# Optimization experiments

Hardware: AMD Instinct MI355X
Metric: run time of the kernel (lower is better)

The kernel has to match this reference:

```python
import jax, jax.numpy as jnp
import numpy as np

D_STATE = 64
HEADDIM = 64
D_CONV = 4
EPS = 1e-5


def _layernorm(x, w, b):
    m = jnp.mean(x, -1, keepdims=True)
    v = jnp.mean((x - m) ** 2, -1, keepdims=True)
    return (x - m) * jax.lax.rsqrt(v + EPS) * w + b


def _mamba2(x, W_in, conv_w, conv_b, dt_bias, A_log, Dh, rms_w, W_out):
    # Mamba2 (SSD) forward: in_proj -> causal depthwise conv + silu -> selective scan
    # -> gated RMSNorm -> out_proj.  ngroups=1, headdim=64, d_state=64.
    Bb, L, _ = x.shape
    d_inner = rms_w.shape[0]
    H = dt_bias.shape[0]
    P = d_inner // H
    conv_dim = d_inner + 2 * D_STATE
    zxbcdt = x @ W_in                                   # [B,L,2*d_inner+2*N+H]
    z = zxbcdt[..., :d_inner]
    xBC = zxbcdt[..., d_inner:d_inner + conv_dim]
    dt = zxbcdt[..., d_inner + conv_dim:]               # [B,L,H]
    # causal depthwise conv1d (kernel D_CONV) + bias + silu
    xpad = jnp.pad(xBC, ((0, 0), (D_CONV - 1, 0), (0, 0)))
    xBC = sum(conv_w[k] * xpad[:, k:k + L] for k in range(D_CONV)) + conv_b
    xBC = jax.nn.silu(xBC)
    xh = xBC[..., :d_inner].reshape(Bb, L, H, P)        # [B,L,H,P]
    Bm = xBC[..., d_inner:d_inner + D_STATE]            # [B,L,N]
    Cm = xBC[..., d_inner + D_STATE:]                   # [B,L,N]
    dt = jax.nn.softplus(dt + dt_bias)                  # [B,L,H]
    A = -jnp.exp(A_log)                                 # [H]
    da = jnp.exp(dt * A)                                # [B,L,H] discrete decay
    dtx = dt[..., None] * xh                            # [B,L,H,P]

    def step(h, inp):
        da_t, dtx_t, B_t, C_t = inp
        h = da_t[:, :, None, None] * h + jnp.einsum('bhp,bn->bhpn', dtx_t, B_t)
        y_t = jnp.einsum('bhpn,bn->bhp', h, C_t)
        return h, y_t

    h0 = jnp.zeros((Bb, H, P, D_STATE), x.dtype)
    _, y = jax.lax.scan(step, h0, (da.transpose(1, 0, 2), dtx.transpose(1, 0, 2, 3),
                                   Bm.transpose(1, 0, 2), Cm.transpose(1, 0, 2)))
    y = y.transpose(1, 0, 2, 3) + Dh[None, None, :, None] * xh   # skip term
    y = y.reshape(Bb, L, d_inner)
    # gated RMSNorm (norm_before_gate=False): rmsnorm(y * silu(z)) * weight
    y = y * jax.nn.silu(z)
    y = y * jax.lax.rsqrt(jnp.mean(y * y, -1, keepdims=True) + EPS) * rms_w
    return y @ W_out


def _mamba_params(key, d_model, pre):
    d_inner = 2 * d_model
    H = d_inner // HEADDIM
    conv_dim = d_inner + 2 * D_STATE
    d_in = 2 * d_inner + 2 * D_STATE + H
    k = jax.random.split(key, 5)
    return {
        pre + '_W_in': jax.random.normal(k[0], (d_model, d_in), jnp.float32) * (d_model ** -0.5),
        pre + '_conv_w': jax.random.normal(k[1], (D_CONV, conv_dim), jnp.float32) * 0.2,
        pre + '_conv_b': jnp.zeros((conv_dim,), jnp.float32),
        pre + '_dt_bias': jnp.log(jnp.expm1(jax.random.uniform(k[2], (H,), jnp.float32, 0.001, 0.1))),
        pre + '_A_log': jnp.log(jax.random.uniform(k[3], (H,), jnp.float32, 1.0, 16.0)),
        pre + '_D': jnp.ones((H,), jnp.float32),
        pre + '_rms_w': jnp.ones((d_inner,), jnp.float32),
        pre + '_W_out': jax.random.normal(k[4], (d_inner, d_model), jnp.float32) * (d_inner ** -0.5),
    }


def setup_inputs() -> dict:
    key = jax.random.key(0)
    ks = jax.random.split(key, 3)
    B, L, C = 8, 1024, 128
    inp = {'x': jax.random.normal(ks[0], (B, L, C), jnp.float32)}
    inp['ln_spa_w'] = jnp.ones((C,), jnp.float32)
    inp['ln_spa_b'] = jnp.zeros((C,), jnp.float32)
    inp['ln_spe_w'] = jnp.ones((L,), jnp.float32)
    inp['ln_spe_b'] = jnp.zeros((L,), jnp.float32)
    inp.update(_mamba_params(ks[1], C, 'spa'))
    inp.update(_mamba_params(ks[2], L, 'spe'))
    return inp


def reference(x, ln_spa_w, ln_spa_b, ln_spe_w, ln_spe_b,
              spa_W_in, spa_conv_w, spa_conv_b, spa_dt_bias, spa_A_log, spa_D, spa_rms_w, spa_W_out,
              spe_W_in, spe_conv_w, spe_conv_b, spe_dt_bias, spe_A_log, spe_D, spe_rms_w, spe_W_out):
    # SSD_Block.forward (drop_path=0 -> identity)
    x_spa = _layernorm(x, ln_spa_w, ln_spa_b)
    x_spa = _mamba2(x_spa, spa_W_in, spa_conv_w, spa_conv_b, spa_dt_bias,
                    spa_A_log, spa_D, spa_rms_w, spa_W_out) + x
    x_spe = x_spa.transpose(0, 2, 1)                      # [B,C,L]
    x_spe = _layernorm(x_spe, ln_spe_w, ln_spe_b)
    x_spe = _mamba2(x_spe, spe_W_in, spe_conv_w, spe_conv_b, spe_dt_bias,
                    spe_A_log, spe_D, spe_rms_w, spe_W_out)
    return x_spe.transpose(0, 2, 1) + x_spa
```

## Files before the change

### kernel.cpp

```cpp
#include <hip/hip_runtime.h>
#include <hip/hip_bf16.h>

#define EPSV 1e-5f

typedef __attribute__((ext_vector_type(8))) short short8v;
typedef __attribute__((ext_vector_type(4))) float f32x4;

__device__ inline unsigned short f2bf(float f) {
  __hip_bfloat16 h = __float2bfloat16(f);
  return *reinterpret_cast<unsigned short*>(&h);
}

__device__ inline float bf2f(unsigned short u) {
  return __uint_as_float(((unsigned int)u) << 16);
}

__device__ inline float siluf(float x) { return x / (1.f + expf(-x)); }

__device__ inline void gload_lds16(const void* g, void* l) {
  __builtin_amdgcn_global_load_lds(
      (const __attribute__((address_space(1))) void*)g,
      (__attribute__((address_space(3))) void*)l, 16, 0, 0);
}

__device__ inline float block_sum(float v, float* lds) {
  #pragma unroll
  for (int o = 32; o; o >>= 1) v += __shfl_xor(v, o);
  int tid = threadIdx.x;
  if ((tid & 63) == 0) lds[tid >> 6] = v;
  __syncthreads();
  float r = lds[0] + lds[1] + lds[2] + lds[3];
  __syncthreads();
  return r;
}

__device__ inline float wave_prefix_incl(float v, int lane) {
  #pragma unroll
  for (int o = 1; o < 64; o <<= 1) {
    float u = __shfl_up(v, o);
    if (lane >= o) v += u;
  }
  return v;
}

__device__ inline void wtconv_tile(const float* __restrict__ W,
                                   unsigned short* __restrict__ Wt,
                                   int K, int N, int bx, int by) {
  __shared__ float tile[64][65];
  int n0 = bx * 64, k0 = by * 64;
  int tid = threadIdx.x;
  int r = tid >> 4, c4 = (tid & 15) * 4;
  #pragma unroll
  for (int i = 0; i < 4; i++) {
    int kk = r + i * 16;
    float4 v = make_float4(0.f, 0.f, 0.f, 0.f);
    if (n0 + c4 < N) v = *reinterpret_cast<const float4*>(&W[(long)(k0 + kk) * N + n0 + c4]);
    tile[kk][c4] = v.x; tile[kk][c4 + 1] = v.y; tile[kk][c4 + 2] = v.z; tile[kk][c4 + 3] = v.w;
  }
  __syncthreads();
  #pragma unroll
  for (int i = 0; i < 4; i++) {
    int nl = r + i * 16;
    if (n0 + nl < N) {
      ushort4 o;
      o.x = f2bf(tile[c4 + 0][nl]);
      o.y = f2bf(tile[c4 + 1][nl]);
      o.z = f2bf(tile[c4 + 2][nl]);
      o.w = f2bf(tile[c4 + 3][nl]);
      *reinterpret_cast<ushort4*>(&Wt[(long)(n0 + nl) * K + k0 + c4]) = o;
    }
  }
}

__global__ __launch_bounds__(256) void ln_wt_fused(const float* __restrict__ x,
                                                   const float* __restrict__ w,
                                                   const float* __restrict__ bb,
                                                   unsigned short* __restrict__ outA,
                                                   const float* __restrict__ W0,
                                                   unsigned short* __restrict__ T0,
                                                   const float* __restrict__ W1,
                                                   unsigned short* __restrict__ T1,
                                                   const float* __restrict__ W2,
                                                   unsigned short* __restrict__ T2,
                                                   const float* __restrict__ W3,
                                                   unsigned short* __restrict__ T3) {
  int id = blockIdx.x;
  if (id < 4096) {
    int tid = threadIdx.x;
    __shared__ float lds[4];
    long row = (long)id * 2 + (tid >> 7);
    int lane = tid & 127;
    int base = (tid >> 7) << 1;
    float v = x[row * 128 + lane];
    float s = v;
    #pragma unroll
    for (int o = 32; o; o >>= 1) s += __shfl_xor(s, o);
    if ((tid & 63) == 0) lds[tid >> 6] = s;
    __syncthreads();
    float m = (lds[base] + lds[base + 1]) * (1.f / 128.f);
    float d = v - m;
    float q = d * d;
    #pragma unroll
    for (int o = 32; o; o >>= 1) q += __shfl_xor(q, o);
    __syncthreads();
    if ((tid & 63) == 0) lds[tid >> 6] = q;
    __syncthreads();
    float inv = rsqrtf((lds[base] + lds[base + 1]) * (1.f / 128.f) + EPSV);
    outA[row * 128 + lane] = f2bf(d * inv * w[lane] + bb[lane]);
  } else {
    id -= 4096;
    if (id < 22)        { int r = id;        wtconv_tile(W0, T0, 128,  644,  r % 11, r / 11); }
    else if (id < 30)   { int r = id - 22;   wtconv_tile(W1, T1, 256,  128,  r % 2,  r / 2); }
    else if (id < 1102) { int r = id - 30;   wtconv_tile(W2, T2, 1024, 4256, r % 67, r / 67); }
    else                { int r = id - 1102; wtconv_tile(W3, T3, 2048, 1024, r % 16, r / 16); }
  }
}

__global__ __launch_bounds__(256) void spe_normT(const float* __restrict__ xspa,
                                                 const float* __restrict__ part2,
                                                 const float* __restrict__ w,
                                                 const float* __restrict__ bb,
                                                 unsigned short* __restrict__ out) {
  __shared__ float tile[128][65];
  int c0 = blockIdx.x * 64, l0 = blockIdx.y * 128, b = blockIdx.z;
  int tid = threadIdx.x;
  int rr = tid >> 4, c4 = (tid & 15) * 4;
  #pragma unroll
  for (int p = 0; p < 8; p++) {
    int l = rr + p * 16;
    f32x4 v = *reinterpret_cast<const f32x4*>(
        &xspa[((long)b * 1024 + l0 + l) * 128 + c0 + c4]);
    tile[l][c4] = v[0]; tile[l][c4 + 1] = v[1];
    tile[l][c4 + 2] = v[2]; tile[l][c4 + 3] = v[3];
  }
  __syncthreads();
  int ch = tid >> 2, lq = tid & 3;
  int gc = c0 + ch;
  int bx = gc >> 6, cl = gc & 63;
  float ssum = 0.f, qsum = 0.f;
  #pragma unroll
  for (int sub = 0; sub < 16; sub++) {
    int by = b * 16 + sub;
    float2 pq = *reinterpret_cast<const float2*>(&part2[(((by * 2 + bx) * 64) + cl) * 2]);
    ssum += pq.x; qsum += pq.y;
  }
  float mm = ssum * (1.f / 1024.f);
  float rstd = rsqrtf(qsum * (1.f / 1024.f) - mm * mm + EPSV);
  #pragma unroll
  for (int j = 0; j < 8; j++) {
    int qidx = lq + j * 4;
    int l = qidx * 4;
    float4 wv = *reinterpret_cast<const float4*>(&w[l0 + l]);
    float4 bv = *reinterpret_cast<const float4*>(&bb[l0 + l]);
    ushort4 o;
    o.x = f2bf((tile[l + 0][ch] - mm) * rstd * wv.x + bv.x);
    o.y = f2bf((tile[l + 1][ch] - mm) * rstd * wv.y + bv.y);
    o.z = f2bf((tile[l + 2][ch] - mm) * rstd * wv.z + bv.z);
    o.w = f2bf((tile[l + 3][ch] - mm) * rstd * wv.w + bv.w);
    *reinterpret_cast<ushort4*>(&out[((long)b * 128 + c0 + ch) * 1024 + l0 + l]) = o;
  }
}

__global__ __launch_bounds__(256) void gemm128_split(const unsigned short* __restrict__ A,
                                                     const unsigned short* __restrict__ Bt,
                                                     unsigned short* __restrict__ zout,
                                                     float* __restrict__ o2,
                                                     float* __restrict__ o3,
                                                     int M, int N, int K,
                                                     int c1, int c2) {
  __shared__ unsigned short As[128 * 32];
  __shared__ unsigned short Bs[128 * 32];
  int tid = threadIdx.x;
  int lane = tid & 63, w = tid >> 6;
  int wr = (w >> 1) * 64, wc = (w & 1) * 64;
  int ln15 = lane & 15, kg = lane >> 4;
  int rowBase = blockIdx.y * 128, colBase = blockIdx.x * 128;
  int srow = w * 32 + (lane >> 2);
  int scol = (lane & 3) * 8;
  f32x4 acc[4][4] = {};
  for (int k0 = 0; k0 < K; k0 += 32) {
    gload_lds16(&A[(long)(rowBase + srow) * K + k0 + scol], &As[(w * 32) * 32]);
    gload_lds16(&A[(long)(rowBase + srow + 16) * K + k0 + scol], &As[(w * 32 + 16) * 32]);
    gload_lds16(&Bt[(long)(colBase + srow) * K + k0 + scol], &Bs[(w * 32) * 32]);
    gload_lds16(&Bt[(long)(colBase + srow + 16) * K + k0 + scol], &Bs[(w * 32 + 16) * 32]);
    __syncthreads();
    short8v af[4], bfr[4];
    #pragma unroll
    for (int mt = 0; mt < 4; mt++)
      af[mt] = *reinterpret_cast<const short8v*>(&As[(wr + mt * 16 + ln15) * 32 + kg * 8]);
    #pragma unroll
    for (int nt = 0; nt < 4; nt++)
      bfr[nt] = *reinterpret_cast<const short8v*>(&Bs[(wc + nt * 16 + ln15) * 32 + kg * 8]);
    #pragma unroll
    for (int mt = 0; mt < 4; mt++)
      #pragma unroll
      for (int nt = 0; nt < 4; nt++)
        acc[mt][nt] = __builtin_amdgcn_mfma_f32_16x16x32_bf16(af[mt], bfr[nt], acc[mt][nt], 0, 0, 0);
    __syncthreads();
  }
  #pragma unroll
  for (int mt = 0; mt < 4; mt++)
    #pragma unroll
    for (int nt = 0; nt < 4; nt++)
      #pragma unroll
      for (int q = 0; q < 4; q++) {
        int r = rowBase + wr + mt * 16 + kg * 4 + q;
        int c = colBase + wc + nt * 16 + ln15;
        if (c < N) {
          float v = acc[mt][nt][q];
          if (c < c1) zout[(long)r * c1 + c] = f2bf(v);
          else if (c < c2) o2[(long)r * (c2 - c1) + (c - c1)] = v;
          else o3[(long)r * (N - c2) + (c - c2)] = v;
        }
      }
}

template <int MODE>
__global__ __launch_bounds__(256) void gemm_mfma(const unsigned short* __restrict__ A,
                                                 const unsigned short* __restrict__ Bt,
                                                 const float* __restrict__ R,
                                                 float* __restrict__ out,
                                                 float* __restrict__ part2,
                                                 int M, int N, int K) {
  __shared__ unsigned short As[64 * 40];
  __shared__ unsigned short Bs[64 * 40];
  int tid = threadIdx.x;
  int lane = tid & 63, w = tid >> 6;
  int wr = (w >> 1) * 32, wc = (w & 1) * 32;
  int ln15 = lane & 15, kg = lane >> 4;
  int rowBase = blockIdx.y * 64, colBase = blockIdx.x * 64;
  int sm = tid >> 2, skb = (tid & 3) * 8;
  f32x4 acc[2][2] = {};
  for (int k0 = 0; k0 < K; k0 += 32) {
    {
      short8v av = *reinterpret_cast<const short8v*>(&A[(long)(rowBase + sm) * K + k0 + skb]);
      *reinterpret_cast<short8v*>(&As[sm * 40 + skb]) = av;
      int n = colBase + sm;
      short8v bv = {0, 0, 0, 0, 0, 0, 0, 0};
      if (n < N) bv = *reinterpret_cast<const short8v*>(&Bt[(long)n * K + k0 + skb]);
      *reinterpret_cast<short8v*>(&Bs[sm * 40 + skb]) = bv;
    }
    __syncthreads();
    short8v af[2], bfr[2];
    #pragma unroll
    for (int mt = 0; mt < 2; mt++)
      af[mt] = *reinterpret_cast<const short8v*>(&As[(wr + mt * 16 + ln15) * 40 + kg * 8]);
    #pragma unroll
    for (int nt = 0; nt < 2; nt++)
      bfr[nt] = *reinterpret_cast<const short8v*>(&Bs[(wc + nt * 16 + ln15) * 40 + kg * 8]);
    #pragma unroll
    for (int mt = 0; mt < 2; mt++)
      #pragma unroll
      for (int nt = 0; nt < 2; nt++)
        acc[mt][nt] = __builtin_amdgcn_mfma_f32_16x16x32_bf16(af[mt], bfr[nt], acc[mt][nt], 0, 0, 0);
    __syncthreads();
  }
  if (MODE == 1) {
    float sC[2] = {0.f, 0.f}, qC[2] = {0.f, 0.f};
    #pragma unroll
    for (int mt = 0; mt < 2; mt++)
      #pragma unroll
      for (int nt = 0; nt < 2; nt++)
        #pragma unroll
        for (int q = 0; q < 4; q++) {
          int r = rowBase + wr + mt * 16 + kg * 4 + q;
          int c = colBase + wc + nt * 16 + ln15;
          float v = acc[mt][nt][q] + R[(long)r * N + c];
          out[(long)r * N + c] = v;
          sC[nt] += v;
          qC[nt] += v * v;
        }
    __shared__ float redS[4][32], redQ[4][32];
    #pragma unroll
    for (int nt = 0; nt < 2; nt++) {
      sC[nt] += __shfl_xor(sC[nt], 16);
      sC[nt] += __shfl_xor(sC[nt], 32);
      qC[nt] += __shfl_xor(qC[nt], 16);
      qC[nt] += __shfl_xor(qC[nt], 32);
    }
    if (lane < 16) {
      redS[w][ln15] = sC[0];       redQ[w][ln15] = qC[0];
      redS[w][16 + ln15] = sC[1];  redQ[w][16 + ln15] = qC[1];
    }
    __syncthreads();
    if (tid < 64) {
      int c = tid;
      int grp = c >> 5, lo = c & 31;
      float ss = redS[grp][lo] + redS[grp + 2][lo];
      float qq = redQ[grp][lo] + redQ[grp + 2][lo];
      long slot = ((long)(blockIdx.y * 2 + blockIdx.x) * 64 + c) * 2;
      part2[slot] = ss;
      part2[slot + 1] = qq;
    }
  } else {
    #pragma unroll
    for (int mt = 0; mt < 2; mt++)
      #pragma unroll
      for (int nt = 0; nt < 2; nt++)
        #pragma unroll
        for (int q = 0; q < 4; q++) {
          int r = rowBase + wr + mt * 16 + kg * 4 + q;
          int c = colBase + wc + nt * 16 + ln15;
          if (c < N) {
            int bb = r >> 7, ch = r & 127;
            out[(long)bb * 131072 + (long)c * 128 + ch] =
                acc[mt][nt][q] + R[((long)bb * 1024 + c) * 128 + ch];
          }
        }
  }
}

__global__ __launch_bounds__(256) void conv_dtda(const float* __restrict__ zx,
                                                 const float* __restrict__ cw,
                                                 const float* __restrict__ cb,
                                                 unsigned short* __restrict__ cout,
                                                 const float* __restrict__ raw,
                                                 const float* __restrict__ dtbias,
                                                 const float* __restrict__ alog,
                                                 float* __restrict__ dt,
                                                 float* __restrict__ la,
                                                 int Bb, int L, int conv_dim,
                                                 int H, int rowsH, int convBlocks) {
  int tid = threadIdx.x;
  if ((int)blockIdx.x < convBlocks) {
    long idx4 = (long)blockIdx.x * 256 + tid;
    int nch4 = conv_dim >> 2;
    long total4 = (long)Bb * L * nch4;
    if (idx4 >= total4) return;
    int ch = (int)(idx4 % nch4) << 2;
    long rt = idx4 / nch4;
    int t = (int)(rt % L);
    int b = (int)(rt / L);
    f32x4 acc = *reinterpret_cast<const f32x4*>(&cb[ch]);
    #pragma unroll
    for (int k = 0; k < 4; k++) {
      int tt = t + k - 3;
      if (tt >= 0) {
        f32x4 wv = *reinterpret_cast<const f32x4*>(&cw[k * conv_dim + ch]);
        f32x4 zv = *reinterpret_cast<const f32x4*>(
            &zx[((long)b * L + tt) * conv_dim + ch]);
        acc += wv * zv;
      }
    }
    ushort4 o;
    o.x = f2bf(siluf(acc[0])); o.y = f2bf(siluf(acc[1]));
    o.z = f2bf(siluf(acc[2])); o.w = f2bf(siluf(acc[3]));
    *reinterpret_cast<ushort4*>(&cout[rt * conv_dim + ch]) = o;
  } else {
    int idx = ((int)blockIdx.x - convBlocks) * 256 + tid;
    if (idx >= rowsH) return;
    int h = idx % H;
    float v = raw[idx] + dtbias[h];
    float sp = (v > 20.f) ? v : log1pf(expf(v));
    dt[idx] = sp;
    la[idx] = -expf(alog[h]) * sp;
  }
}

__global__ __launch_bounds__(256) void ssd_local(const unsigned short* __restrict__ xbc,
                                                 const float* __restrict__ dtv,
                                                 const float* __restrict__ la,
                                                 float* __restrict__ Sc,
                                                 float* __restrict__ Aprod,
                                                 int NC, int nc_launch, int H,
                                                 int conv_dim, int d_inner) {
  int blk = blockIdx.x;
  int c = blk % nc_launch, bh = blk / nc_launch;
  int h = bh % H, b = bh / H;
  int tid = threadIdx.x;
  long row0 = ((long)(b * NC + c)) * 64;
  __shared__ unsigned short XpT[64 * 72];
  __shared__ unsigned short BT[64 * 72];
  __shared__ float Ws[64];
  int tq = tid >> 4, cq = (tid & 15) << 2;
  ushort4 xr[4], br[4];
  #pragma unroll
  for (int i = 0; i < 4; i++) {
    int t = tq + i * 16;
    const unsigned short* rp = xbc + (row0 + t) * conv_dim;
    xr[i] = *reinterpret_cast<const ushort4*>(rp + (h << 6) + cq);
    br[i] = *reinterpret_cast<const ushort4*>(rp + d_inner + cq);
  }
  if (tid < 64) {
    long r = (row0 + tid) * H + h;
    float cum = wave_prefix_incl(la[r], tid);
    float cT = __shfl(cum, 63);
    Ws[tid] = expf(cT - cum) * dtv[r];
    if (tid == 63) Aprod[(long)bh * NC + c] = expf(cT);
  }
  __syncthreads();
  #pragma unroll
  for (int i = 0; i < 4; i++) {
    int t = tq + i * 16;
    float wv = Ws[t];
    XpT[(cq + 0) * 72 + t] = f2bf(wv * bf2f(xr[i].x));
    XpT[(cq + 1) * 72 + t] = f2bf(wv * bf2f(xr[i].y));
    XpT[(cq + 2) * 72 + t] = f2bf(wv * bf2f(xr[i].z));
    XpT[(cq + 3) * 72 + t] = f2bf(wv * bf2f(xr[i].w));
    BT[(cq + 0) * 72 + t] = br[i].x;
    BT[(cq + 1) * 72 + t] = br[i].y;
    BT[(cq + 2) * 72 + t] = br[i].z;
    BT[(cq + 3) * 72 + t] = br[i].w;
  }
  __syncthreads();
  int lane = tid & 63, wv2 = tid >> 6;
  int wr = (wv2 >> 1) * 32, wc = (wv2 & 1) * 32;
  int ln15 = lane & 15, kg = lane >> 4;
  f32x4 acc[2][2] = {};
  #pragma unroll
  for (int ks = 0; ks < 2; ks++) {
    short8v af[2], bq[2];
    #pragma unroll
    for (int mt = 0; mt < 2; mt++)
      af[mt] = *reinterpret_cast<const short8v*>(&XpT[(wr + mt * 16 + ln15) * 72 + ks * 32 + kg * 8]);
    #pragma unroll
    for (int nt = 0; nt < 2; nt++)
      bq[nt] = *reinterpret_cast<const short8v*>(&BT[(wc + nt * 16 + ln15) * 72 + ks * 32 + kg * 8]);
    #pragma unroll
    for (int mt = 0; mt < 2; mt++)
      #pragma unroll
      for (int nt = 0; nt < 2; nt++)
        acc[mt][nt] = __builtin_amdgcn_mfma_f32_16x16x32_bf16(af[mt], bq[nt], acc[mt][nt], 0, 0, 0);
  }
  float* base = Sc + ((long)bh * NC + c) * 4096;
  #pragma unroll
  for (int mt = 0; mt < 2; mt++)
    #pragma unroll
    for (int nt = 0; nt < 2; nt++)
      #pragma unroll
      for (int q = 0; q < 4; q++) {
        int p = wr + mt * 16 + kg * 4 + q;
        int n = wc + nt * 16 + ln15;
        base[p * 64 + n] = acc[mt][nt][q];
      }
}

__global__ __launch_bounds__(256) void ssd_out(const unsigned short* __restrict__ xbc,
                                               const float* __restrict__ dtv,
                                               const float* __restrict__ la,
                                               const float* __restrict__ Sc,
                                               const float* __restrict__ Aprod,
                                               const float* __restrict__ Dvec,
                                               unsigned short* __restrict__ y,
                                               int NC, int H, int conv_dim,
                                               int d_inner) {
  int blk = blockIdx.x;
  int c = blk % NC, bh = blk / NC;
  int h = bh % H, b = bh / H;
  int tid = threadIdx.x;
  long row0 = ((long)(b * NC + c)) * 64;
  __shared__ unsigned short Cb[64 * 72];
  __shared__ unsigned short Bb[64 * 72];
  __shared__ unsigned short XT[64 * 72];
  __shared__ unsigned short hb[64 * 72];
  __shared__ float Cum[64], Dt[64];
  int tq = tid >> 4, cq = (tid & 15) << 2;
  #pragma unroll
  for (int i = 0; i < 4; i++) {
    int t = tq + i * 16;
    const unsigned short* rp = xbc + (row0 + t) * conv_dim;
    ushort4 cu = *reinterpret_cast<const ushort4*>(rp + d_inner + 64 + cq);
    ushort4 bu = *reinterpret_cast<const ushort4*>(rp + d_inner + cq);
    ushort4 xu = *reinterpret_cast<const ushort4*>(rp + (h << 6) + cq);
    *reinterpret_cast<ushort4*>(&Cb[t * 72 + cq]) = cu;
    *reinterpret_cast<ushort4*>(&Bb[t * 72 + cq]) = bu;
    XT[(cq + 0) * 72 + t] = xu.x;
    XT[(cq + 1) * 72 + t] = xu.y;
    XT[(cq + 2) * 72 + t] = xu.z;
    XT[(cq + 3) * 72 + t] = xu.w;
  }
  if (c > 0) {
    f32x4 hreg[4] = {};
    const float* ap = Aprod + (long)bh * NC;
    for (int j = 0; j < c; j++) {
      const float* sb = Sc + ((long)bh * NC + j) * 4096;
      float a = ap[j];
      #pragma unroll
      for (int i = 0; i < 4; i++) {
        int p = tq + i * 16;
        f32x4 sv = *reinterpret_cast<const f32x4*>(&sb[p * 64 + cq]);
        hreg[i] = hreg[i] * a + sv;
      }
    }
    #pragma unroll
    for (int i = 0; i < 4; i++) {
      int p = tq + i * 16;
      ushort4 ho;
      ho.x = f2bf(hreg[i][0]); ho.y = f2bf(hreg[i][1]);
      ho.z = f2bf(hreg[i][2]); ho.w = f2bf(hreg[i][3]);
      *reinterpret_cast<ushort4*>(&hb[p * 72 + cq]) = ho;
    }
  }
  if (tid < 64) {
    long r = (row0 + tid) * H + h;
    Cum[tid] = wave_prefix_incl(la[r], tid);
    Dt[tid] = dtv[r];
  }
  __syncthreads();
  int lane = tid & 63, wv2 = tid >> 6;
  int wr = (wv2 >> 1) * 32, wc = (wv2 & 1) * 32;
  int ln15 = lane & 15, kg = lane >> 4;
  f32x4 accA[2][2] = {};
  #pragma unroll
  for (int ks = 0; ks < 2; ks++) {
    short8v af[2], bq[2];
    #pragma unroll
    for (int mt = 0; mt < 2; mt++)
      af[mt] = *reinterpret_cast<const short8v*>(&Cb[(wr + mt * 16 + ln15) * 72 + ks * 32 + kg * 8]);
    #pragma unroll
    for (int nt = 0; nt < 2; nt++)
      bq[nt] = *reinterpret_cast<const short8v*>(&Bb[(wc + nt * 16 + ln15) * 72 + ks * 32 + kg * 8]);
    #pragma unroll
    for (int mt = 0; mt < 2; mt++)
      #pragma unroll
      for (int nt = 0; nt < 2; nt++)
        accA[mt][nt] = __builtin_amdgcn_mfma_f32_16x16x32_bf16(af[mt], bq[nt], accA[mt][nt], 0, 0, 0);
  }
  unsigned short gmb[2][2][4];
  #pragma unroll
  for (int mt = 0; mt < 2; mt++)
    #pragma unroll
    for (int nt = 0; nt < 2; nt++)
      #pragma unroll
      for (int q = 0; q < 4; q++) {
        int t = wr + mt * 16 + kg * 4 + q;
        int s = wc + nt * 16 + ln15;
        float v = (s <= t) ? accA[mt][nt][q] * expf(Cum[t] - Cum[s]) * Dt[s] : 0.f;
        gmb[mt][nt][q] = f2bf(v);
      }
  __syncthreads();
  #pragma unroll
  for (int mt = 0; mt < 2; mt++)
    #pragma unroll
    for (int nt = 0; nt < 2; nt++)
      #pragma unroll
      for (int q = 0; q < 4; q++)
        Bb[(wr + mt * 16 + kg * 4 + q) * 72 + wc + nt * 16 + ln15] = gmb[mt][nt][q];
  __syncthreads();
  f32x4 accY[2][2] = {}, accZ[2][2] = {};
  #pragma unroll
  for (int ks = 0; ks < 2; ks++) {
    short8v af[2], bq[2];
    #pragma unroll
    for (int mt = 0; mt < 2; mt++)
      af[mt] = *reinterpret_cast<const short8v*>(&Bb[(wr + mt * 16 + ln15) * 72 + ks * 32 + kg * 8]);
    #pragma unroll
    for (int nt = 0; nt < 2; nt++)
      bq[nt] = *reinterpret_cast<const short8v*>(&XT[(wc + nt * 16 + ln15) * 72 + ks * 32 + kg * 8]);
    #pragma unroll
    for (int mt = 0; mt < 2; mt++)
      #pragma unroll
      for (int nt = 0; nt < 2; nt++)
        accY[mt][nt] = __builtin_amdgcn_mfma_f32_16x16x32_bf16(af[mt], bq[nt], accY[mt][nt], 0, 0, 0);
  }
  if (c > 0) {
    #pragma unroll
    for (int ks = 0; ks < 2; ks++) {
      short8v af[2], bq[2];
      #pragma unroll
      for (int mt = 0; mt < 2; mt++)
        af[mt] = *reinterpret_cast<const short8v*>(&Cb[(wr + mt * 16 + ln15) * 72 + ks * 32 + kg * 8]);
      #pragma unroll
      for (int nt = 0; nt < 2; nt++)
        bq[nt] = *reinterpret_cast<const short8v*>(&hb[(wc + nt * 16 + ln15) * 72 + ks * 32 + kg * 8]);
      #pragma unroll
      for (int mt = 0; mt < 2; mt++)
        #pragma unroll
        for (int nt = 0; nt < 2; nt++)
          accZ[mt][nt] = __builtin_amdgcn_mfma_f32_16x16x32_bf16(af[mt], bq[nt], accZ[mt][nt], 0, 0, 0);
    }
  }
  float Dv = Dvec[h];
  #pragma unroll
  for (int mt = 0; mt < 2; mt++)
    #pragma unroll
    for (int q = 0; q < 4; q++) {
      int t = wr + mt * 16 + kg * 4 + q;
      float wB = expf(Cum[t]);
      const unsigned short* xp = xbc + (row0 + t) * conv_dim + (h << 6);
      unsigned short* yp = y + (row0 + t) * d_inner + (h << 6);
      #pragma unroll
      for (int nt = 0; nt < 2; nt++) {
        int p = wc + nt * 16 + ln15;
        yp[p] = f2bf(accY[mt][nt][q] + accZ[mt][nt][q] * wB + bf2f(xp[p]) * Dv);
      }
    }
}

template <int CPL>
__global__ __launch_bounds__(256) void gate_rms_bf16(const unsigned short* __restrict__ y,
                                                     const unsigned short* __restrict__ z,
                                                     const float* __restrict__ rmsw,
                                                     unsigned short* __restrict__ ab,
                                                     int d_inner) {
  long row = (long)blockIdx.x * 4 + (threadIdx.x >> 6);
  int lane = threadIdx.x & 63;
  const unsigned short* yr = y + row * d_inner;
  const unsigned short* zr = z + row * d_inner;
  float g[CPL];
  float ss = 0.f;
  #pragma unroll
  for (int j = 0; j < CPL / 4; j++) {
    int c = j * 256 + lane * 4;
    ushort4 yv = *reinterpret_cast<const ushort4*>(&yr[c]);
    ushort4 zv = *reinterpret_cast<const ushort4*>(&zr[c]);
    float g0 = bf2f(yv.x) * siluf(bf2f(zv.x));
    float g1 = bf2f(yv.y) * siluf(bf2f(zv.y));
    float g2 = bf2f(yv.z) * siluf(bf2f(zv.z));
    float g3 = bf2f(yv.w) * siluf(bf2f(zv.w));
    g[j * 4 + 0] = g0; g[j * 4 + 1] = g1; g[j * 4 + 2] = g2; g[j * 4 + 3] = g3;
    ss += g0 * g0 + g1 * g1 + g2 * g2 + g3 * g3;
  }
  #pragma unroll
  for (int o = 32; o; o >>= 1) ss += __shfl_xor(ss, o);
  float inv = rsqrtf(ss / (float)d_inner + EPSV);
  #pragma unroll
  for (int j = 0; j < CPL / 4; j++) {
    int c = j * 256 + lane * 4;
    float4 wv = *reinterpret_cast<const float4*>(&rmsw[c]);
    ushort4 o;
    o.x = f2bf(g[j * 4 + 0] * inv * wv.x);
    o.y = f2bf(g[j * 4 + 1] * inv * wv.y);
    o.z = f2bf(g[j * 4 + 2] * inv * wv.z);
    o.w = f2bf(g[j * 4 + 3] * inv * wv.w);
    *reinterpret_cast<ushort4*>(&ab[row * d_inner + c]) = o;
  }
}

extern "C" void kernel_launch(void* const* d_in, const int* in_sizes, int n_in,
                              void* d_out, int out_size, void* d_ws,
                              size_t ws_size, hipStream_t stream) {
  const float* x        = (const float*)d_in[0];
  const float* ln_spa_w = (const float*)d_in[1];
  const float* ln_spa_b = (const float*)d_in[2];
  const float* ln_spe_w = (const float*)d_in[3];
  const float* ln_spe_b = (const float*)d_in[4];
  const float* spa_W_in   = (const float*)d_in[5];
  const float* spa_conv_w = (const float*)d_in[6];
  const float* spa_conv_b = (const float*)d_in[7];
  const float* spa_dt_b   = (const float*)d_in[8];
  const float* spa_A_log  = (const float*)d_in[9];
  const float* spa_D      = (const float*)d_in[10];
  const float* spa_rms_w  = (const float*)d_in[11];
  const float* spa_W_out  = (const float*)d_in[12];
  const float* spe_W_in   = (const float*)d_in[13];
  const float* spe_conv_w = (const float*)d_in[14];
  const float* spe_conv_b = (const float*)d_in[15];
  const float* spe_dt_b   = (const float*)d_in[16];
  const float* spe_A_log  = (const float*)d_in[17];
  const float* spe_D      = (const float*)d_in[18];
  const float* spe_rms_w  = (const float*)d_in[19];
  const float* spe_W_out  = (const float*)d_in[20];
  float* out = (float*)d_out;

  float* ws = (float*)d_ws;
  float* xspa   = ws;
  unsigned short* z = (unsigned short*)(ws + 1048576);
  float* xbcraw = ws + 3145728;
  float* dtraw  = ws + 6291456;
  unsigned short* cv = (unsigned short*)(ws + 6324224);
  float* dtb    = ws + 9469952;
  float* la     = ws + 9502720;
  unsigned short* yb = (unsigned short*)(ws + 9535488);
  unsigned short* Abf     = (unsigned short*)(ws + 11634688);
  unsigned short* Wt_spai = (unsigned short*)(ws + 12683264);
  unsigned short* Wt_spao = (unsigned short*)(ws + 12724480);
  unsigned short* Wt_spei = (unsigned short*)(ws + 12740864);
  unsigned short* Wt_speo = (unsigned short*)(ws + 14919936);

  hipLaunchKernelGGL(ln_wt_fused, dim3(5710), dim3(256), 0, stream,
                     x, ln_spa_w, ln_spa_b, Abf,
                     spa_W_in, Wt_spai, spa_W_out, Wt_spao,
                     spe_W_in, Wt_spei, spe_W_out, Wt_speo);

  hipLaunchKernelGGL(gemm128_split, dim3(6, 64), dim3(256), 0, stream,
                     Abf, Wt_spai, z, xbcraw, dtraw,
                     8192, 644, 128, 256, 640);
  hipLaunchKernelGGL(conv_dtda, dim3(3200), dim3(256), 0, stream,
                     xbcraw, spa_conv_w, spa_conv_b, cv,
                     dtraw, spa_dt_b, spa_A_log, dtb, la,
                     8, 1024, 384, 4, 32768, 3072);
  hipLaunchKernelGGL(ssd_local, dim3(480), dim3(256), 0, stream,
                     cv, dtb, la, xbcraw, dtraw, 16, 15, 4, 384, 256);
  hipLaunchKernelGGL(ssd_out, dim3(512), dim3(256), 0, stream,
                     cv, dtb, la, xbcraw, dtraw, spa_D, yb, 16, 4, 384, 256);
  hipLaunchKernelGGL((gate_rms_bf16<4>), dim3(2048), dim3(256), 0, stream,
                     yb, z, spa_rms_w, Abf, 256);
  hipLaunchKernelGGL((gemm_mfma<1>), dim3(2, 128), dim3(256), 0, stream,
                     Abf, Wt_spao, x, xspa, dtb, 8192, 128, 256);

  hipLaunchKernelGGL(spe_normT, dim3(2, 8, 8), dim3(256), 0, stream,
                     xspa, dtb, ln_spe_w, ln_spe_b, Abf);
  hipLaunchKernelGGL(gemm128_split, dim3(34, 8), dim3(256), 0, stream,
                     Abf, Wt_spei, z, xbcraw, dtraw,
                     1024, 4256, 1024, 2048, 4224);
  hipLaunchKernelGGL(conv_dtda, dim3(2304), dim3(256), 0, stream,
                     xbcraw, spe_conv_w, spe_conv_b, cv,
                     dtraw, spe_dt_b, spe_A_log, dtb, la,
                     8, 128, 2176, 32, 32768, 2176);
  hipLaunchKernelGGL(ssd_local, dim3(256), dim3(256), 0, stream,
                     cv, dtb, la, xbcraw, dtraw, 2, 1, 32, 2176, 2048);
  hipLaunchKernelGGL(ssd_out, dim3(512), dim3(256), 0, stream,
                     cv, dtb, la, xbcraw, dtraw, spe_D, yb, 2, 32, 2176, 2048);
  hipLaunchKernelGGL((gate_rms_bf16<32>), dim3(256), dim3(256), 0, stream,
                     yb, z, spe_rms_w, Abf, 2048);
  hipLaunchKernelGGL((gemm_mfma<2>), dim3(16, 16), dim3(256), 0, stream,
                     Abf, Wt_speo, xspa, out, nullptr, 1024, 1024, 2048);
}
```

Before: 173.7 us.

## Store conv input in bf16 and use 128x64 tiled GEMM for spectral out-proj

The in-projection GEMM now writes the xBC conv-input slice as bf16 rather than fp32, and the conv kernel reads bf16 and widens to float, halving that intermediate's traffic. The buffer region previously aliased by the scan state is reused through a separate float pointer. The spectral out-projection GEMM moves from a 64x64 tile kernel to a 128x64 tile using direct global-to-LDS loads with fewer blocks. The trade is precision loss on the conv input and fewer blocks (128) for the final GEMM, which may underfill the GPU.

```diff
diff --git a/kernel.cpp b/kernel.cpp
--- a/kernel.cpp
+++ b/kernel.cpp
@@ -164,7 +164,7 @@
 __global__ __launch_bounds__(256) void gemm128_split(const unsigned short* __restrict__ A,
                                                      const unsigned short* __restrict__ Bt,
                                                      unsigned short* __restrict__ zout,
-                                                     float* __restrict__ o2,
+                                                     unsigned short* __restrict__ o2,
                                                      float* __restrict__ o3,
                                                      int M, int N, int K,
                                                      int c1, int c2) {
@@ -209,19 +209,67 @@
         if (c < N) {
           float v = acc[mt][nt][q];
           if (c < c1) zout[(long)r * c1 + c] = f2bf(v);
-          else if (c < c2) o2[(long)r * (c2 - c1) + (c - c1)] = v;
+          else if (c < c2) o2[(long)r * (c2 - c1) + (c - c1)] = f2bf(v);
           else o3[(long)r * (N - c2) + (c - c2)] = v;
         }
       }
 }
 
-template <int MODE>
-__global__ __launch_bounds__(256) void gemm_mfma(const unsigned short* __restrict__ A,
-                                                 const unsigned short* __restrict__ Bt,
-                                                 const float* __restrict__ R,
-                                                 float* __restrict__ out,
-                                                 float* __restrict__ part2,
-                                                 int M, int N, int K) {
+__global__ __launch_bounds__(256) void gemm128x64_t(const unsigned short* __restrict__ A,
+                                                    const unsigned short* __restrict__ Bt,
+                                                    const float* __restrict__ R,
+                                                    float* __restrict__ out,
+                                                    int M, int N, int K) {
+  __shared__ unsigned short As[128 * 32];
+  __shared__ unsigned short Bs[64 * 32];
+  int tid = threadIdx.x;
+  int lane = tid & 63, w = tid >> 6;
+  int wr = w * 32;
+  int ln15 = lane & 15, kg = lane >> 4;
+  int rowBase = blockIdx.y * 128, colBase = blockIdx.x * 64;
+  int arow = w * 32 + (lane >> 2);
+  int brow = w * 16 + (lane >> 2);
+  int scol = (lane & 3) * 8;
+  f32x4 acc[2][4] = {};
+  for (int k0 = 0; k0 < K; k0 += 32) {
+    gload_lds16(&A[(long)(rowBase + arow) * K + k0 + scol], &As[(w * 32) * 32]);
+    gload_lds16(&A[(long)(rowBase + arow + 16) * K + k0 + scol], &As[(w * 32 + 16) * 32]);
+    gload_lds16(&Bt[(long)(colBase + brow) * K + k0 + scol], &Bs[(w * 16) * 32]);
+    __syncthreads();
+    short8v af[2], bfr[4];
+    #pragma unroll
+    for (int mt = 0; mt < 2; mt++)
+      af[mt] = *reinterpret_cast<const short8v*>(&As[(wr + mt * 16 + ln15) * 32 + kg * 8]);
+    #pragma unroll
+    for (int nt = 0; nt < 4; nt++)
+      bfr[nt] = *reinterpret_cast<const short8v*>(&Bs[(nt * 16 + ln15) * 32 + kg * 8]);
+    #pragma unroll
+    for (int mt = 0; mt < 2; mt++)
+      #pragma unroll
+      for (int nt = 0; nt < 4; nt++)
+        acc[mt][nt] = __builtin_amdgcn_mfma_f32_16x16x32_bf16(af[mt], bfr[nt], acc[mt][nt], 0, 0, 0);
+    __syncthreads();
+  }
+  #pragma unroll
+  for (int mt = 0; mt < 2; mt++)
+    #pragma unroll
+    for (int nt = 0; nt < 4; nt++)
+      #pragma unroll
+      for (int q = 0; q < 4; q++) {
+        int r = rowBase + wr + mt * 16 + kg * 4 + q;
+        int c = colBase + nt * 16 + ln15;
+        int bb = r >> 7, ch = r & 127;
+        out[(long)bb * 131072 + (long)c * 128 + ch] =
+            acc[mt][nt][q] + R[((long)bb * 1024 + c) * 128 + ch];
+      }
+}
+
+__global__ __launch_bounds__(256) void gemm_mfma1(const unsigned short* __restrict__ A,
+                                                  const unsigned short* __restrict__ Bt,
+                                                  const float* __restrict__ R,
+                                                  float* __restrict__ out,
+                                                  float* __restrict__ part2,
+                                                  int M, int N, int K) {
   __shared__ unsigned short As[64 * 40];
   __shared__ unsigned short Bs[64 * 40];
   int tid = threadIdx.x;
@@ -255,62 +303,45 @@
         acc[mt][nt] = __builtin_amdgcn_mfma_f32_16x16x32_bf16(af[mt], bfr[nt], acc[mt][nt], 0, 0, 0);
     __syncthreads();
   }
-  if (MODE == 1) {
-    float sC[2] = {0.f, 0.f}, qC[2] = {0.f, 0.f};
-    #pragma unroll
-    for (int mt = 0; mt < 2; mt++)
-      #pragma unroll
-      for (int nt = 0; nt < 2; nt++)
-        #pragma unroll
-        for (int q = 0; q < 4; q++) {
-          int r = rowBase + wr + mt * 16 + kg * 4 + q;
-          int c = colBase + wc + nt * 16 + ln15;
-          float v = acc[mt][nt][q] + R[(long)r * N + c];
-          out[(long)r * N + c] = v;
-          sC[nt] += v;
-          qC[nt] += v * v;
-        }
-    __shared__ float redS[4][32], redQ[4][32];
-    #pragma unroll
-    for (int nt = 0; nt < 2; nt++) {
-      sC[nt] += __shfl_xor(sC[nt], 16);
-      sC[nt] += __shfl_xor(sC[nt], 32);
-      qC[nt] += __shfl_xor(qC[nt], 16);
-      qC[nt] += __shfl_xor(qC[nt], 32);
-    }
-    if (lane < 16) {
-      redS[w][ln15] = sC[0];       redQ[w][ln15] = qC[0];
-      redS[w][16 + ln15] = sC[1];  redQ[w][16 + ln15] = qC[1];
-    }
-    __syncthreads();
-    if (tid < 64) {
-      int c = tid;
-      int grp = c >> 5, lo = c & 31;
-      float ss = redS[grp][lo] + redS[grp + 2][lo];
-      float qq = redQ[grp][lo] + redQ[grp + 2][lo];
-      long slot = ((long)(blockIdx.y * 2 + blockIdx.x) * 64 + c) * 2;
-      part2[slot] = ss;
-      part2[slot + 1] = qq;
-    }
-  } else {
-    #pragma unroll
-    for (int mt = 0; mt < 2; mt++)
-      #pragma unroll
-      for (int nt = 0; nt < 2; nt++)
-        #pragma unroll
-        for (int q = 0; q < 4; q++) {
-          int r = rowBase + wr + mt * 16 + kg * 4 + q;
-          int c = colBase + wc + nt * 16 + ln15;
-          if (c < N) {
-            int bb = r >> 7, ch = r & 127;
-            out[(long)bb * 131072 + (long)c * 128 + ch] =
-                acc[mt][nt][q] + R[((long)bb * 1024 + c) * 128 + ch];
-          }
-        }
-  }
-}
-
-__global__ __launch_bounds__(256) void conv_dtda(const float* __restrict__ zx,
+  float sC[2] = {0.f, 0.f}, qC[2] = {0.f, 0.f};
+  #pragma unroll
+  for (int mt = 0; mt < 2; mt++)
+    #pragma unroll
+    for (int nt = 0; nt < 2; nt++)
+      #pragma unroll
+      for (int q = 0; q < 4; q++) {
+        int r = rowBase + wr + mt * 16 + kg * 4 + q;
+        int c = colBase + wc + nt * 16 + ln15;
+        float v = acc[mt][nt][q] + R[(long)r * N + c];
+        out[(long)r * N + c] = v;
+        sC[nt] += v;
+        qC[nt] += v * v;
+      }
+  __shared__ float redS[4][32], redQ[4][32];
+  #pragma unroll
+  for (int nt = 0; nt < 2; nt++) {
+    sC[nt] += __shfl_xor(sC[nt], 16);
+    sC[nt] += __shfl_xor(sC[nt], 32);
+    qC[nt] += __shfl_xor(qC[nt], 16);
+    qC[nt] += __shfl_xor(qC[nt], 32);
+  }
+  if (lane < 16) {
+    redS[w][ln15] = sC[0];       redQ[w][ln15] = qC[0];
+    redS[w][16 + ln15] = sC[1];  redQ[w][16 + ln15] = qC[1];
+  }
+  __syncthreads();
+  if (tid < 64) {
+    int c = tid;
+    int grp = c >> 5, lo = c & 31;
+    float ss = redS[grp][lo] + redS[grp + 2][lo];
+    float qq = redQ[grp][lo] + redQ[grp + 2][lo];
+    long slot = ((long)(blockIdx.y * 2 + blockIdx.x) * 64 + c) * 2;
+    part2[slot] = ss;
+    part2[slot + 1] = qq;
+  }
+}
+
+__global__ __launch_bounds__(256) void conv_dtda(const unsigned short* __restrict__ zx,
                                                  const float* __restrict__ cw,
                                                  const float* __restrict__ cb,
                                                  unsigned short* __restrict__ cout,
@@ -337,9 +368,12 @@
       int tt = t + k - 3;
       if (tt >= 0) {
         f32x4 wv = *reinterpret_cast<const f32x4*>(&cw[k * conv_dim + ch]);
-        f32x4 zv = *reinterpret_cast<const f32x4*>(
+        ushort4 zu = *reinterpret_cast<const ushort4*>(
             &zx[((long)b * L + tt) * conv_dim + ch]);
-        acc += wv * zv;
+        acc[0] += wv[0] * bf2f(zu.x);
+        acc[1] += wv[1] * bf2f(zu.y);
+        acc[2] += wv[2] * bf2f(zu.z);
+        acc[3] += wv[3] * bf2f(zu.w);
       }
     }
     ushort4 o;
@@ -656,7 +690,8 @@
   float* ws = (float*)d_ws;
   float* xspa   = ws;
   unsigned short* z = (unsigned short*)(ws + 1048576);
-  float* xbcraw = ws + 3145728;
+  unsigned short* xbcraw = (unsigned short*)(ws + 3145728);
+  float* Sc     = ws + 3145728;
   float* dtraw  = ws + 6291456;
   unsigned short* cv = (unsigned short*)(ws + 6324224);
   float* dtb    = ws + 9469952;
@@ -681,12 +716,12 @@
                      dtraw, spa_dt_b, spa_A_log, dtb, la,
                      8, 1024, 384, 4, 32768, 3072);
   hipLaunchKernelGGL(ssd_local, dim3(480), dim3(256), 0, stream,
-                     cv, dtb, la, xbcraw, dtraw, 16, 15, 4, 384, 256);
+                     cv, dtb, la, Sc, dtraw, 16, 15, 4, 384, 256);
   hipLaunchKernelGGL(ssd_out, dim3(512), dim3(256), 0, stream,
-                     cv, dtb, la, xbcraw, dtraw, spa_D, yb, 16, 4, 384, 256);
+                     cv, dtb, la, Sc, dtraw, spa_D, yb, 16, 4, 384, 256);
   hipLaunchKernelGGL((gate_rms_bf16<4>), dim3(2048), dim3(256), 0, stream,
                      yb, z, spa_rms_w, Abf, 256);
-  hipLaunchKernelGGL((gemm_mfma<1>), dim3(2, 128), dim3(256), 0, stream,
+  hipLaunchKernelGGL(gemm_mfma1, dim3(2, 128), dim3(256), 0, stream,
                      Abf, Wt_spao, x, xspa, dtb, 8192, 128, 256);
 
   hipLaunchKernelGGL(spe_normT, dim3(2, 8, 8), dim3(256), 0, stream,
@@ -699,11 +734,11 @@
                      dtraw, spe_dt_b, spe_A_log, dtb, la,
                      8, 128, 2176, 32, 32768, 2176);
   hipLaunchKernelGGL(ssd_local, dim3(256), dim3(256), 0, stream,
-                     cv, dtb, la, xbcraw, dtraw, 2, 1, 32, 2176, 2048);
+                     cv, dtb, la, Sc, dtraw, 2, 1, 32, 2176, 2048);
   hipLaunchKernelGGL(ssd_out, dim3(512), dim3(256), 0, stream,
-                     cv, dtb, la, xbcraw, dtraw, spe_D, yb, 2, 32, 2176, 2048);
+                     cv, dtb, la, Sc, dtraw, spe_D, yb, 2, 32, 2176, 2048);
   hipLaunchKernelGGL((gate_rms_bf16<32>), dim3(256), dim3(256), 0, stream,
                      yb, z, spe_rms_w, Abf, 2048);
-  hipLaunchKernelGGL((gemm_mfma<2>), dim3(16, 16), dim3(256), 0, stream,
-                     Abf, Wt_speo, xspa, out, nullptr, 1024, 1024, 2048);
-}
+  hipLaunchKernelGGL(gemm128x64_t, dim3(16, 8), dim3(256), 0, stream,
+                     Abf, Wt_speo, xspa, out, 1024, 1024, 2048);
+}
```

New measurement: 166.6 us. 4.1% less time.
